# Optimization experiments

Measured on AMD Instinct MI355X. Metric: run time of the kernel, lower is better.

The kernel has to match this reference:

```python
import jax, jax.numpy as jnp
import numpy as np

N = 100_000   # nodes
E = 1_600_000 # edges (avg degree 16)
G = 1_000     # graphs in batch
IN = 3
H = 64
EPS = 1e-5    # BatchNorm eps


def setup_inputs() -> dict:
    key = jax.random.key(0)
    ks = jax.random.split(key, 16)
    x = jax.random.normal(ks[0], (N, IN), jnp.float32)
    edge_index = jax.random.randint(ks[1], (2, E), 0, N, dtype=jnp.int64)
    # sorted segment ids covering every graph (no empty segments for max-pool)
    batch = (jnp.arange(N, dtype=jnp.int64) * G) // N
    s = 0.1
    return {
        "x": x,
        "edge_index": edge_index,
        "batch": batch,
        "W0": jax.random.normal(ks[2], (IN, H), jnp.float32) * s,
        "b0": jax.random.normal(ks[3], (H,), jnp.float32) * s,
        "W_hidden": jax.random.normal(ks[4], (2, H, H), jnp.float32) * s,
        "b_hidden": jax.random.normal(ks[5], (2, H), jnp.float32) * s,
        "bn_gamma": jax.random.uniform(ks[6], (3, H), jnp.float32, 0.5, 1.5),
        "bn_beta": jax.random.normal(ks[7], (3, H), jnp.float32) * s,
        "bn_mean": jax.random.normal(ks[8], (3, H), jnp.float32) * s,
        "bn_var": jax.random.uniform(ks[9], (3, H), jnp.float32, 0.5, 1.5),
        "fc1_W": jax.random.normal(ks[10], (2 * H, 128), jnp.float32) * s,
        "fc1_b": jnp.zeros((128,), jnp.float32),
        "fc2_W": jax.random.normal(ks[11], (128, 64), jnp.float32) * s,
        "fc2_b": jnp.zeros((64,), jnp.float32),
        "fcg_W": jax.random.normal(ks[12], (64, 1), jnp.float32) * s,
        "fcg_b": jnp.zeros((1,), jnp.float32),
        "fcb_W": jax.random.normal(ks[13], (64, 1), jnp.float32) * s,
        "fcb_b": jnp.zeros((1,), jnp.float32),
    }


def _gcn_conv(h, W, b, src, dst, dinv):
    """PyG GCNConv: self-loops + symmetric deg^{-1/2} normalization."""
    hw = h @ W                                   # [N, out]
    norm = dinv[src] * dinv[dst]                 # [E]
    agg = jax.ops.segment_sum(hw[src] * norm[:, None], dst, num_segments=N)
    # self-loop contribution: norm_ii = dinv_i^2
    return agg + hw * (dinv * dinv)[:, None] + b


def reference(x, edge_index, batch, W0, b0, W_hidden, b_hidden,
              bn_gamma, bn_beta, bn_mean, bn_var,
              fc1_W, fc1_b, fc2_W, fc2_b, fcg_W, fcg_b, fcb_W, fcb_b):
    src, dst = edge_index[0], edge_index[1]
    # degree including self-loop, computed on target nodes (PyG gcn_norm)
    deg = jax.ops.segment_sum(jnp.ones((E,), x.dtype), dst, num_segments=N) + 1.0
    dinv = jax.lax.rsqrt(deg)

    h = x
    for i in range(3):
        W = W0 if i == 0 else W_hidden[i - 1]
        b = b0 if i == 0 else b_hidden[i - 1]
        hn = _gcn_conv(h, W, b, src, dst, dinv)
        # BatchNorm1d (eval mode, running stats) + ReLU; dropout = identity in eval
        hn = (hn - bn_mean[i]) * jax.lax.rsqrt(bn_var[i] + EPS) * bn_gamma[i] + bn_beta[i]
        hn = jax.nn.relu(hn)
        h = h + hn if (i > 0 and h.shape[1] == hn.shape[1]) else hn

    # segment pooling over graphs
    counts = jax.ops.segment_sum(jnp.ones((N,), h.dtype), batch, num_segments=G)
    x_mean = jax.ops.segment_sum(h, batch, num_segments=G) / counts[:, None]
    x_max = jax.ops.segment_max(h, batch, num_segments=G)
    g = jnp.concatenate([x_mean, x_max], axis=1)     # [G, 2H]

    g = jax.nn.relu(g @ fc1_W + fc1_b)
    g = jax.nn.relu(g @ fc2_W + fc2_b)
    gamma = g @ fcg_W + fcg_b
    beta = g @ fcb_W + fcb_b
    return jnp.concatenate([gamma, beta], axis=1)    # [G, 2*p_layers]
```

## Files before the change

### kernel.cpp

```cpp
#include <hip/hip_runtime.h>
#include <hip/hip_fp16.h>
#include <math.h>
#include <float.h>

#define EPSBN 1e-5f
#define NBK   200
#define CAPB  9728
#define STGB  64
#define BATCH 4096


__global__ void zero_cursors(int* __restrict__ cursors) {
    if (threadIdx.x < NBK) cursors[threadIdx.x] = 0;
}

__global__ void bin_edges(const int* __restrict__ src, const int* __restrict__ dst,
                          int* __restrict__ bufs, int* __restrict__ cursors,
                          int E, int N) {
    __shared__ int stage[NBK * STGB];
    __shared__ int cnt[NBK];
    __shared__ int bpos[NBK];
    int tid = threadIdx.x;
    int nb = (N + 511) >> 9;

    int chunk = (((E + gridDim.x - 1) / gridDim.x) + 3) & ~3;
    int e0 = blockIdx.x * chunk;
    int e1 = min(e0 + chunk, E);

    for (int base = e0; base < e1; base += BATCH) {
        for (int i = tid; i < NBK; i += 512) cnt[i] = 0;
        __syncthreads();

#pragma unroll
        for (int it = 0; it < 2; it++) {
            int e = base + it * 2048 + tid * 4;
            if (e + 4 <= e1) {
                int4 d4 = *(const int4*)(dst + e);
                int4 s4 = *(const int4*)(src + e);
                int dd[4] = {d4.x, d4.y, d4.z, d4.w};
                int ss[4] = {s4.x, s4.y, s4.z, s4.w};
#pragma unroll
                for (int q = 0; q < 4; q++) {
                    int d = dd[q];
                    int b = d >> 9;
                    int w = ((d & 511) << 17) | ss[q];
                    int pos = atomicAdd(&cnt[b], 1);
                    if (pos < STGB) stage[b * STGB + pos] = w;
                }
            } else {
                for (int qq = e; qq < e1 && qq < e + 4; qq++) {
                    int d = dst[qq];
                    int b = d >> 9;
                    int w = ((d & 511) << 17) | src[qq];
                    int pos = atomicAdd(&cnt[b], 1);
                    if (pos < STGB) stage[b * STGB + pos] = w;
                }
            }
        }
        __syncthreads();
        if (tid < nb) bpos[tid] = atomicAdd(&cursors[tid], min(cnt[tid], STGB));
        __syncthreads();
        int wv = tid >> 6, ln = tid & 63;
        for (int b = wv; b < nb; b += 8) {
            int c = min(cnt[b], STGB), bp = bpos[b];
            int* dstp = bufs + (size_t)b * CAPB + bp;
            for (int i = ln; i < c; i += 64)
                if (bp + i < CAPB) dstp[i] = stage[b * STGB + i];
        }
        __syncthreads();
    }
}

__global__ void __launch_bounds__(512)
build_csr(const int* __restrict__ bufs, const int* __restrict__ cursors,
          const float* __restrict__ x,
          float* __restrict__ dinv, float* __restrict__ xs,
          int* __restrict__ off0, int* __restrict__ off1,
          int* __restrict__ csr, int N) {
    __shared__ int cnt[512];
    __shared__ int pfx[512];
    __shared__ unsigned sorted[CAPB];
    int tid = threadIdx.x;
    int b = blockIdx.x;
    cnt[tid] = 0;
    __syncthreads();
    int total = min(cursors[b], CAPB);
    const int* buf = bufs + (size_t)b * CAPB;

    for (int i = tid * 4; i + 4 <= total; i += 2048) {
        int4 w4 = *(const int4*)(buf + i);
        atomicAdd(&cnt[w4.x >> 17], 1);
        atomicAdd(&cnt[w4.y >> 17], 1);
        atomicAdd(&cnt[w4.z >> 17], 1);
        atomicAdd(&cnt[w4.w >> 17], 1);
    }
    for (int i = (total & ~3) + tid; i < total; i += 512)
        atomicAdd(&cnt[buf[i] >> 17], 1);
    __syncthreads();

    int v = cnt[tid];
    pfx[tid] = v;
    __syncthreads();
    for (int off = 1; off < 512; off <<= 1) {
        int t = (tid >= off) ? pfx[tid - off] : 0;
        __syncthreads();
        pfx[tid] += t;
        __syncthreads();
    }
    int excl = pfx[tid] - v;
    int gbase = b * CAPB;
    int gi = (b << 9) + tid;
    if (gi < N) {
        float di = 1.0f / sqrtf((float)v + 1.0f);
        dinv[gi] = di;
        off0[gi] = gbase + excl;
        off1[gi] = gbase + excl + v;
        xs[gi * 3]     = x[gi * 3]     * di;
        xs[gi * 3 + 1] = x[gi * 3 + 1] * di;
        xs[gi * 3 + 2] = x[gi * 3 + 2] * di;
    }
    cnt[tid] = excl;
    __syncthreads();

    for (int i = tid * 4; i + 4 <= total; i += 2048) {
        int4 w4 = *(const int4*)(buf + i);
        int ww[4] = {w4.x, w4.y, w4.z, w4.w};
#pragma unroll
        for (int q = 0; q < 4; q++) {
            int pos = atomicAdd(&cnt[ww[q] >> 17], 1);
            sorted[pos] = (unsigned)(ww[q] & 0x1FFFF);
        }
    }
    for (int i = (total & ~3) + tid; i < total; i += 512) {
        int w = buf[i];
        int pos = atomicAdd(&cnt[w >> 17], 1);
        sorted[pos] = (unsigned)(w & 0x1FFFF);
    }
    __syncthreads();

    for (int i = tid; i < total; i += 512)
        csr[gbase + i] = (int)sorted[i];
}

__global__ void agg3(const float* __restrict__ xs, const float* __restrict__ dinv,
                     const int* __restrict__ csr,
                     const int* __restrict__ off0, const int* __restrict__ off1,
                     float* __restrict__ ax, int N) {
    int n = blockIdx.x * blockDim.x + threadIdx.x;
    if (n >= N) return;
    float a0 = xs[n * 3], a1 = xs[n * 3 + 1], a2 = xs[n * 3 + 2];
    float b0 = 0.f, b1 = 0.f, b2 = 0.f;
    int e0 = off0[n], e1 = off1[n];
    int e = e0;
    for (; e + 4 <= e1; e += 4) {
        int s0 = csr[e] * 3, s1 = csr[e + 1] * 3, s2 = csr[e + 2] * 3, s3 = csr[e + 3] * 3;
        float x00 = xs[s0], x01 = xs[s0 + 1], x02 = xs[s0 + 2];
        float x10 = xs[s1], x11 = xs[s1 + 1], x12 = xs[s1 + 2];
        float x20 = xs[s2], x21 = xs[s2 + 1], x22 = xs[s2 + 2];
        float x30 = xs[s3], x31 = xs[s3 + 1], x32 = xs[s3 + 2];
        a0 += x00 + x20; a1 += x01 + x21; a2 += x02 + x22;
        b0 += x10 + x30; b1 += x11 + x31; b2 += x12 + x32;
    }
    for (; e < e1; e++) {
        int s = csr[e] * 3;
        a0 += xs[s]; a1 += xs[s + 1]; a2 += xs[s + 2];
    }
    float di = dinv[n];
    ax[n * 3]     = (a0 + b0) * di;
    ax[n * 3 + 1] = (a1 + b1) * di;
    ax[n * 3 + 2] = (a2 + b2) * di;
}

__global__ void mm_bn(const float* __restrict__ ax, const float* __restrict__ W,
                      const float* __restrict__ b,
                      const float* __restrict__ bng, const float* __restrict__ bnb,
                      const float* __restrict__ bnm, const float* __restrict__ bnv,
                      __half* __restrict__ h, int N) {
    int t = blockIdx.x * blockDim.x + threadIdx.x;
    int n = t >> 6, f = t & 63;
    if (n < N) {
        float a = ax[n * 3] * W[f] + ax[n * 3 + 1] * W[64 + f]
                + ax[n * 3 + 2] * W[128 + f] + b[f];
        float v = (a - bnm[f]) * rsqrtf(bnv[f] + EPSBN) * bng[f] + bnb[f];
        v = fmaxf(v, 0.f);
        float other = __shfl_xor(v, 1, 64);
        if (!(f & 1)) ((__half2*)h)[t >> 1] = __floats2half2_rn(v, other);
    }
}

__global__ void mm64_reg(const __half* __restrict__ h, const float* __restrict__ W,
                         const float* __restrict__ dinv, __half* __restrict__ hw, int N) {
    int tid = threadIdx.x;
    int lane = tid & 63;
    int wave = blockIdx.x * (blockDim.x >> 6) + (tid >> 6);
    int nwaves = gridDim.x * (blockDim.x >> 6);

    float wcol[64];
#pragma unroll
    for (int k = 0; k < 64; k++) wcol[k] = W[k * 64 + lane];

    for (int n = wave; n < N; n += nwaves) {
        float hval = __half2float(h[(size_t)n * 64 + lane]);
        float a0 = 0.f, a1 = 0.f, a2 = 0.f, a3 = 0.f;
#pragma unroll
        for (int k = 0; k < 64; k += 4) {
            float b0 = __int_as_float(__builtin_amdgcn_readlane(__float_as_int(hval), k));
            float b1 = __int_as_float(__builtin_amdgcn_readlane(__float_as_int(hval), k + 1));
            float b2 = __int_as_float(__builtin_amdgcn_readlane(__float_as_int(hval), k + 2));
            float b3 = __int_as_float(__builtin_amdgcn_readlane(__float_as_int(hval), k + 3));
            a0 += b0 * wcol[k];
            a1 += b1 * wcol[k + 1];
            a2 += b2 * wcol[k + 2];
            a3 += b3 * wcol[k + 3];
        }
        float res = ((a0 + a1) + (a2 + a3)) * dinv[n];
        float other = __shfl_xor(res, 1, 64);
        if (!(lane & 1))
            ((__half2*)hw)[((size_t)n * 64 + lane) >> 1] = __floats2half2_rn(res, other);
    }
}


__device__ inline void acc8(float* a, uint4 r) {
    const __half2* p = (const __half2*)&r;
#pragma unroll
    for (int j = 0; j < 4; j++) {
        float2 f = __half22float2(p[j]);
        a[2 * j] += f.x;
        a[2 * j + 1] += f.y;
    }
}

__global__ void agg_bn(const uint4* __restrict__ hw4, __half* __restrict__ h,
                       const float* __restrict__ dinv,
                       const int* __restrict__ csr,
                       const int* __restrict__ off0, const int* __restrict__ off1,
                       const float4* __restrict__ bias4,
                       const float4* __restrict__ gamma4, const float4* __restrict__ beta4,
                       const float4* __restrict__ mean4, const float4* __restrict__ var4,
                       int N) {
    int tid = threadIdx.x;
    int n = blockIdx.x * 32 + (tid >> 3);
    int f8 = tid & 7;
    if (n >= N) return;

    float a0[8], a1[8], a2[8], a3[8];
#pragma unroll
    for (int j = 0; j < 8; j++) { a0[j] = 0.f; a1[j] = 0.f; a2[j] = 0.f; a3[j] = 0.f; }
    acc8(a0, hw4[(size_t)n * 8 + f8]);

    int e0 = off0[n], e1 = off1[n];
    int e = e0;
    for (; e + 8 <= e1; e += 8) {
        int s0 = csr[e],     s1 = csr[e + 1], s2 = csr[e + 2], s3 = csr[e + 3];
        int s4 = csr[e + 4], s5 = csr[e + 5], s6 = csr[e + 6], s7 = csr[e + 7];
        uint4 v0 = hw4[(size_t)s0 * 8 + f8];
        uint4 v1 = hw4[(size_t)s1 * 8 + f8];
        uint4 v2 = hw4[(size_t)s2 * 8 + f8];
        uint4 v3 = hw4[(size_t)s3 * 8 + f8];
        uint4 v4 = hw4[(size_t)s4 * 8 + f8];
        uint4 v5 = hw4[(size_t)s5 * 8 + f8];
        uint4 v6 = hw4[(size_t)s6 * 8 + f8];
        uint4 v7 = hw4[(size_t)s7 * 8 + f8];
        acc8(a0, v0); acc8(a1, v1); acc8(a2, v2); acc8(a3, v3);
        acc8(a0, v4); acc8(a1, v5); acc8(a2, v6); acc8(a3, v7);
    }
    for (; e + 4 <= e1; e += 4) {
        int s0 = csr[e], s1 = csr[e + 1], s2 = csr[e + 2], s3 = csr[e + 3];
        uint4 v0 = hw4[(size_t)s0 * 8 + f8];
        uint4 v1 = hw4[(size_t)s1 * 8 + f8];
        uint4 v2 = hw4[(size_t)s2 * 8 + f8];
        uint4 v3 = hw4[(size_t)s3 * 8 + f8];
        acc8(a0, v0); acc8(a1, v1); acc8(a2, v2); acc8(a3, v3);
    }
    for (; e < e1; e++)
        acc8(a0, hw4[(size_t)csr[e] * 8 + f8]);

    float di = dinv[n];
    float4 bA = bias4[f8 * 2],  bB = bias4[f8 * 2 + 1];
    float4 gA = gamma4[f8 * 2], gB = gamma4[f8 * 2 + 1];
    float4 eA = beta4[f8 * 2],  eB = beta4[f8 * 2 + 1];
    float4 mA = mean4[f8 * 2],  mB = mean4[f8 * 2 + 1];
    float4 vA = var4[f8 * 2],   vB = var4[f8 * 2 + 1];
    float bb[8] = {bA.x, bA.y, bA.z, bA.w, bB.x, bB.y, bB.z, bB.w};
    float gg[8] = {gA.x, gA.y, gA.z, gA.w, gB.x, gB.y, gB.z, gB.w};
    float ee[8] = {eA.x, eA.y, eA.z, eA.w, eB.x, eB.y, eB.z, eB.w};
    float mm[8] = {mA.x, mA.y, mA.z, mA.w, mB.x, mB.y, mB.z, mB.w};
    float vv[8] = {vA.x, vA.y, vA.z, vA.w, vB.x, vB.y, vB.z, vB.w};

    float r[8];
#pragma unroll
    for (int j = 0; j < 8; j++) {
        float acc = (a0[j] + a1[j]) + (a2[j] + a3[j]);
        float t = (acc * di + bb[j] - mm[j]) * (1.0f / sqrtf(vv[j] + EPSBN)) * gg[j] + ee[j];
        r[j] = fmaxf(t, 0.f);
    }
    {
        uint4 hp = ((const uint4*)h)[(size_t)n * 8 + f8];
        const __half2* pp = (const __half2*)&hp;
#pragma unroll
        for (int j = 0; j < 4; j++) {
            float2 f = __half22float2(pp[j]);
            r[2 * j] += f.x;
            r[2 * j + 1] += f.y;
        }
    }
    uint4 outv;
    __half2* po = (__half2*)&outv;
#pragma unroll
    for (int j = 0; j < 4; j++) po[j] = __floats2half2_rn(r[2 * j], r[2 * j + 1]);
    ((uint4*)h)[(size_t)n * 8 + f8] = outv;
}


__device__ inline float4 h4_to_f4(uint2 r) {
    __half2 a = *(__half2*)&r.x;
    __half2 b = *(__half2*)&r.y;
    float2 fa = __half22float2(a), fb = __half22float2(b);
    return make_float4(fa.x, fa.y, fb.x, fb.y);
}

__global__ void __launch_bounds__(256)
pool_mlp(const uint2* __restrict__ h2, const int* __restrict__ batch, int N,
         const float* __restrict__ W1, const float* __restrict__ b1,
         const float* __restrict__ W2, const float* __restrict__ b2,
         const float* __restrict__ Wg, const float* __restrict__ bg,
         const float* __restrict__ Wb, const float* __restrict__ bbv,
         float* __restrict__ out) {
    __shared__ float4 ssum[256], smax[256];
    __shared__ float pooled[128];
    __shared__ float h1[128], hh2[64];
    __shared__ int range[2];
    int g = blockIdx.x;
    int tid = threadIdx.x;

    if (tid < 2) {
        int target = g + tid;
        int lo = 0, hi = N;
        while (lo < hi) {
            int mid = (lo + hi) >> 1;
            if (batch[mid] < target) lo = mid + 1; else hi = mid;
        }
        range[tid] = lo;
    }
    __syncthreads();
    int s = range[0], e = range[1];

    int f4 = tid & 15, c = tid >> 4;
    float4 sum = make_float4(0.f, 0.f, 0.f, 0.f);
    float4 mx = make_float4(-FLT_MAX, -FLT_MAX, -FLT_MAX, -FLT_MAX);
    for (int i = s + c; i < e; i += 16) {
        float4 v = h4_to_f4(h2[(size_t)i * 16 + f4]);
        sum.x += v.x; sum.y += v.y; sum.z += v.z; sum.w += v.w;
        mx.x = fmaxf(mx.x, v.x); mx.y = fmaxf(mx.y, v.y);
        mx.z = fmaxf(mx.z, v.z); mx.w = fmaxf(mx.w, v.w);
    }
    ssum[tid] = sum;
    smax[tid] = mx;
    __syncthreads();
    for (int half = 8; half >= 1; half >>= 1) {
        if (c < half) {
            int o = tid + half * 16;
            ssum[tid].x += ssum[o].x; ssum[tid].y += ssum[o].y;
            ssum[tid].z += ssum[o].z; ssum[tid].w += ssum[o].w;
            smax[tid].x = fmaxf(smax[tid].x, smax[o].x);
            smax[tid].y = fmaxf(smax[tid].y, smax[o].y);
            smax[tid].z = fmaxf(smax[tid].z, smax[o].z);
            smax[tid].w = fmaxf(smax[tid].w, smax[o].w);
        }
        __syncthreads();
    }
    if (c == 0) {
        float inv = 1.0f / (float)(e - s);
        float4 S = ssum[tid], M = smax[tid];
        pooled[f4 * 4 + 0] = S.x * inv;
        pooled[f4 * 4 + 1] = S.y * inv;
        pooled[f4 * 4 + 2] = S.z * inv;
        pooled[f4 * 4 + 3] = S.w * inv;
        pooled[64 + f4 * 4 + 0] = M.x;
        pooled[64 + f4 * 4 + 1] = M.y;
        pooled[64 + f4 * 4 + 2] = M.z;
        pooled[64 + f4 * 4 + 3] = M.w;
    }
    __syncthreads();

    if (tid < 128) {
        float acc = b1[tid];
#pragma unroll 8
        for (int k = 0; k < 128; k++) acc += pooled[k] * W1[k * 128 + tid];
        h1[tid] = fmaxf(acc, 0.0f);
    }
    __syncthreads();
    if (tid < 64) {
        float a2 = b2[tid];
#pragma unroll 8
        for (int k = 0; k < 128; k++) a2 += h1[k] * W2[k * 64 + tid];
        hh2[tid] = fmaxf(a2, 0.0f);
    }
    __syncthreads();
    if (tid < 2) {
        const float* Wv = (tid == 0) ? Wg : Wb;
        float a = (tid == 0) ? bg[0] : bbv[0];
        for (int k = 0; k < 64; k++) a += hh2[k] * Wv[k];
        out[g * 2 + tid] = a;
    }
}


extern "C" void kernel_launch(void* const* d_in, const int* in_sizes, int n_in,
                              void* d_out, int out_size, void* d_ws, size_t ws_size,
                              hipStream_t stream) {
    const float* x    = (const float*)d_in[0];
    const int*   ei   = (const int*)d_in[1];
    const int*   batch= (const int*)d_in[2];
    const float* W0   = (const float*)d_in[3];
    const float* b0   = (const float*)d_in[4];
    const float* Wh   = (const float*)d_in[5];
    const float* bh   = (const float*)d_in[6];
    const float* bng  = (const float*)d_in[7];
    const float* bnb  = (const float*)d_in[8];
    const float* bnm  = (const float*)d_in[9];
    const float* bnv  = (const float*)d_in[10];
    const float* fc1W = (const float*)d_in[11];
    const float* fc1b = (const float*)d_in[12];
    const float* fc2W = (const float*)d_in[13];
    const float* fc2b = (const float*)d_in[14];
    const float* fcgW = (const float*)d_in[15];
    const float* fcgb = (const float*)d_in[16];
    const float* fcbW = (const float*)d_in[17];
    const float* fcbb = (const float*)d_in[18];
    float* out = (float*)d_out;

    const int N = in_sizes[0] / 3;
    const int E = in_sizes[1] / 2;
    const int G = out_size / 2;
    const int* src = ei;
    const int* dst = ei + E;
    const int nb = (N + 511) >> 9;

    char* ws = (char*)d_ws;
    auto alloc = [&](size_t bytes) {
        char* p = ws;
        ws += (bytes + 255) & ~(size_t)255;
        return p;
    };
    float*  dinv    = (float*)alloc((size_t)N * 4);
    int*    off0    = (int*)alloc((size_t)N * 4);
    int*    off1    = (int*)alloc((size_t)N * 4);
    int*    csr     = (int*)alloc((size_t)NBK * CAPB * 4);
    int*    bufs    = (int*)alloc((size_t)NBK * CAPB * 4);
    int*    cursors = (int*)alloc(NBK * 4);
    float*  xs      = (float*)alloc((size_t)N * 3 * 4);
    float*  ax      = (float*)alloc((size_t)N * 3 * 4);
    __half* h       = (__half*)alloc((size_t)N * 64 * 2);
    __half* hw      = (__half*)alloc((size_t)N * 64 * 2);

    const int B = 256;

    zero_cursors<<<1, 256, 0, stream>>>(cursors);
    bin_edges<<<768, 512, 0, stream>>>(src, dst, bufs, cursors, E, N);
    build_csr<<<nb, 512, 0, stream>>>(bufs, cursors, x, dinv, xs, off0, off1, csr, N);

    int aggBlocks = (N + 31) / 32;

    agg3<<<(N + B - 1) / B, B, 0, stream>>>(xs, dinv, csr, off0, off1, ax, N);
    mm_bn<<<((size_t)N * 64 + B - 1) / B, B, 0, stream>>>(ax, W0, b0,
                                                          bng, bnb, bnm, bnv, h, N);
    mm64_reg<<<1024, 256, 0, stream>>>(h, Wh, dinv, hw, N);
    agg_bn<<<aggBlocks, 256, 0, stream>>>((const uint4*)hw, h, dinv, csr, off0, off1,
                                          (const float4*)(bh),
                                          (const float4*)(bng + 64), (const float4*)(bnb + 64),
                                          (const float4*)(bnm + 64), (const float4*)(bnv + 64), N);
    mm64_reg<<<1024, 256, 0, stream>>>(h, Wh + 4096, dinv, hw, N);
    agg_bn<<<aggBlocks, 256, 0, stream>>>((const uint4*)hw, h, dinv, csr, off0, off1,
                                          (const float4*)(bh + 64),
                                          (const float4*)(bng + 128), (const float4*)(bnb + 128),
                                          (const float4*)(bnm + 128), (const float4*)(bnv + 128), N);

    pool_mlp<<<G, 256, 0, stream>>>((const uint2*)h, batch, N,
                                    fc1W, fc1b, fc2W, fc2b,
                                    fcgW, fcgb, fcbW, fcbb, out);
}
```

Measured before the change: 320.4 us.

## Use MFMA with split fp16 weights for 64x64 GEMM and widen gather unroll

Replaces the readlane-based per-node 64x64 matmul with an MFMA 16x16x32 f16 kernel. The fp32 weights are split into hi and lo fp16 halves in a prep kernel, which also zeroes the cursors, so accuracy stays close to fp32. Output tiles are staged through LDS so each row is written with coalesced 16-byte stores. The aggregation loop is also unrolled to 16 outstanding gathers to raise memory-level parallelism, at the cost of more registers.

```diff
diff --git a/kernel.cpp b/kernel.cpp
--- a/kernel.cpp
+++ b/kernel.cpp
@@ -9,9 +9,21 @@
 #define STGB  64
 #define BATCH 4096
 
-
-__global__ void zero_cursors(int* __restrict__ cursors) {
-    if (threadIdx.x < NBK) cursors[threadIdx.x] = 0;
+typedef _Float16 f16x8 __attribute__((ext_vector_type(8)));
+typedef float f32x4 __attribute__((ext_vector_type(4)));
+
+
+__global__ void prep(const float* __restrict__ W, __half* __restrict__ Whi,
+                     __half* __restrict__ Wlo, int n, int* __restrict__ cursors) {
+    int i = blockIdx.x * 256 + threadIdx.x;
+    if (blockIdx.x == 0 && threadIdx.x < NBK) cursors[threadIdx.x] = 0;
+    if (i < n) {
+        float w = W[i];
+        __half hi = __float2half_rn(w);
+        float rem = w - __half2float(hi);
+        Whi[i] = hi;
+        Wlo[i] = __float2half_rn(rem);
+    }
 }
 
 __global__ void bin_edges(const int* __restrict__ src, const int* __restrict__ dst,
@@ -188,35 +200,72 @@
     }
 }
 
-__global__ void mm64_reg(const __half* __restrict__ h, const float* __restrict__ W,
-                         const float* __restrict__ dinv, __half* __restrict__ hw, int N) {
+__global__ void __launch_bounds__(256)
+mm64_mfma(const __half* __restrict__ hH, const __half* __restrict__ WhiH,
+          const __half* __restrict__ WloH, const float* __restrict__ dinv,
+          __half* __restrict__ hw, int N) {
+    __shared__ _Float16 lds[4][16 * 68];
+    const _Float16* Whi = (const _Float16*)WhiH;
+    const _Float16* Wlo = (const _Float16*)WloH;
+    const _Float16* hh  = (const _Float16*)hH;
+
     int tid = threadIdx.x;
     int lane = tid & 63;
-    int wave = blockIdx.x * (blockDim.x >> 6) + (tid >> 6);
-    int nwaves = gridDim.x * (blockDim.x >> 6);
-
-    float wcol[64];
-#pragma unroll
-    for (int k = 0; k < 64; k++) wcol[k] = W[k * 64 + lane];
-
-    for (int n = wave; n < N; n += nwaves) {
-        float hval = __half2float(h[(size_t)n * 64 + lane]);
-        float a0 = 0.f, a1 = 0.f, a2 = 0.f, a3 = 0.f;
-#pragma unroll
-        for (int k = 0; k < 64; k += 4) {
-            float b0 = __int_as_float(__builtin_amdgcn_readlane(__float_as_int(hval), k));
-            float b1 = __int_as_float(__builtin_amdgcn_readlane(__float_as_int(hval), k + 1));
-            float b2 = __int_as_float(__builtin_amdgcn_readlane(__float_as_int(hval), k + 2));
-            float b3 = __int_as_float(__builtin_amdgcn_readlane(__float_as_int(hval), k + 3));
-            a0 += b0 * wcol[k];
-            a1 += b1 * wcol[k + 1];
-            a2 += b2 * wcol[k + 2];
-            a3 += b3 * wcol[k + 3];
-        }
-        float res = ((a0 + a1) + (a2 + a3)) * dinv[n];
-        float other = __shfl_xor(res, 1, 64);
-        if (!(lane & 1))
-            ((__half2*)hw)[((size_t)n * 64 + lane) >> 1] = __floats2half2_rn(res, other);
+    int wv = tid >> 6;
+    int col = lane & 15;
+    int q = lane >> 4;
+    int gwave = blockIdx.x * 4 + wv;
+    int nwaves = gridDim.x * 4;
+    int ntiles = (N + 15) >> 4;
+
+    f16x8 Bh[2][4], Bl[2][4];
+#pragma unroll
+    for (int t = 0; t < 2; t++)
+#pragma unroll
+        for (int g = 0; g < 4; g++) {
+#pragma unroll
+            for (int j = 0; j < 8; j++) {
+                int k = t * 32 + q * 8 + j;
+                Bh[t][g][j] = Whi[k * 64 + g * 16 + col];
+                Bl[t][g][j] = Wlo[k * 64 + g * 16 + col];
+            }
+        }
+
+    _Float16* sl = lds[wv];
+
+    for (int tile = gwave; tile < ntiles; tile += nwaves) {
+        int base = tile << 4;
+        int arow = base + col;
+        if (arow > N - 1) arow = N - 1;
+        f32x4 acc[4] = {};
+#pragma unroll
+        for (int t = 0; t < 2; t++) {
+            f16x8 a = *(const f16x8*)(hh + (size_t)arow * 64 + t * 32 + q * 8);
+#pragma unroll
+            for (int g = 0; g < 4; g++) {
+                acc[g] = __builtin_amdgcn_mfma_f32_16x16x32_f16(a, Bh[t][g], acc[g], 0, 0, 0);
+                acc[g] = __builtin_amdgcn_mfma_f32_16x16x32_f16(a, Bl[t][g], acc[g], 0, 0, 0);
+            }
+        }
+#pragma unroll
+        for (int r = 0; r < 4; r++) {
+            int row = base + q * 4 + r;
+            float di = dinv[row < N ? row : N - 1];
+#pragma unroll
+            for (int g = 0; g < 4; g++)
+                sl[(q * 4 + r) * 68 + g * 16 + col] = (_Float16)(acc[g][r] * di);
+        }
+        asm volatile("s_waitcnt lgkmcnt(0)" ::: "memory");
+#pragma unroll
+        for (int p = 0; p < 2; p++) {
+            int row = (lane >> 3) + p * 8;
+            int ck = lane & 7;
+            uint4 v = *(const uint4*)(sl + row * 68 + ck * 8);
+            int grow = base + row;
+            if (grow < N)
+                *(uint4*)(hw + (size_t)grow * 64 + ck * 8) = v;
+        }
+        asm volatile("s_waitcnt lgkmcnt(0)" ::: "memory");
     }
 }
 
@@ -251,19 +300,17 @@
 
     int e0 = off0[n], e1 = off1[n];
     int e = e0;
-    for (; e + 8 <= e1; e += 8) {
-        int s0 = csr[e],     s1 = csr[e + 1], s2 = csr[e + 2], s3 = csr[e + 3];
-        int s4 = csr[e + 4], s5 = csr[e + 5], s6 = csr[e + 6], s7 = csr[e + 7];
-        uint4 v0 = hw4[(size_t)s0 * 8 + f8];
-        uint4 v1 = hw4[(size_t)s1 * 8 + f8];
-        uint4 v2 = hw4[(size_t)s2 * 8 + f8];
-        uint4 v3 = hw4[(size_t)s3 * 8 + f8];
-        uint4 v4 = hw4[(size_t)s4 * 8 + f8];
-        uint4 v5 = hw4[(size_t)s5 * 8 + f8];
-        uint4 v6 = hw4[(size_t)s6 * 8 + f8];
-        uint4 v7 = hw4[(size_t)s7 * 8 + f8];
-        acc8(a0, v0); acc8(a1, v1); acc8(a2, v2); acc8(a3, v3);
-        acc8(a0, v4); acc8(a1, v5); acc8(a2, v6); acc8(a3, v7);
+    for (; e + 16 <= e1; e += 16) {
+        int s[16];
+#pragma unroll
+        for (int j = 0; j < 16; j++) s[j] = csr[e + j];
+        uint4 v[16];
+#pragma unroll
+        for (int j = 0; j < 16; j++) v[j] = hw4[(size_t)s[j] * 8 + f8];
+#pragma unroll
+        for (int j = 0; j < 16; j += 4) {
+            acc8(a0, v[j]); acc8(a1, v[j + 1]); acc8(a2, v[j + 2]); acc8(a3, v[j + 3]);
+        }
     }
     for (; e + 4 <= e1; e += 4) {
         int s0 = csr[e], s1 = csr[e + 1], s2 = csr[e + 2], s3 = csr[e + 3];
@@ -454,10 +501,12 @@
     float*  ax      = (float*)alloc((size_t)N * 3 * 4);
     __half* h       = (__half*)alloc((size_t)N * 64 * 2);
     __half* hw      = (__half*)alloc((size_t)N * 64 * 2);
+    __half* whi     = (__half*)alloc(2 * 4096 * 2);
+    __half* wlo     = (__half*)alloc(2 * 4096 * 2);
 
     const int B = 256;
 
-    zero_cursors<<<1, 256, 0, stream>>>(cursors);
+    prep<<<32, 256, 0, stream>>>(Wh, whi, wlo, 8192, cursors);
     bin_edges<<<768, 512, 0, stream>>>(src, dst, bufs, cursors, E, N);
     build_csr<<<nb, 512, 0, stream>>>(bufs, cursors, x, dinv, xs, off0, off1, csr, N);
 
@@ -466,12 +515,12 @@
     agg3<<<(N + B - 1) / B, B, 0, stream>>>(xs, dinv, csr, off0, off1, ax, N);
     mm_bn<<<((size_t)N * 64 + B - 1) / B, B, 0, stream>>>(ax, W0, b0,
                                                           bng, bnb, bnm, bnv, h, N);
-    mm64_reg<<<1024, 256, 0, stream>>>(h, Wh, dinv, hw, N);
+    mm64_mfma<<<784, 256, 0, stream>>>(h, whi, wlo, dinv, hw, N);
     agg_bn<<<aggBlocks, 256, 0, stream>>>((const uint4*)hw, h, dinv, csr, off0, off1,
                                           (const float4*)(bh),
                                           (const float4*)(bng + 64), (const float4*)(bnb + 64),
                                           (const float4*)(bnm + 64), (const float4*)(bnv + 64), N);
-    mm64_reg<<<1024, 256, 0, stream>>>(h, Wh + 4096, dinv, hw, N);
+    mm64_mfma<<<784, 256, 0, stream>>>(h, whi + 4096, wlo + 4096, dinv, hw, N);
     agg_bn<<<aggBlocks, 256, 0, stream>>>((const uint4*)hw, h, dinv, csr, off0, off1,
                                           (const float4*)(bh + 64),
                                           (const float4*)(bng + 128), (const float4*)(bnb + 128),
```

After: 277.3 us. 13.5% less time.
